# Optimization experiments

Measured on AMD Instinct MI355X. Metric: run time of the kernel, lower is better.

## Reference

```python
import jax, jax.numpy as jnp
import numpy as np
import math

B, T = 32, 64
VOCAB = 50005
EMB = 512
HID = 1024
SES = 1024
KNOW = 8785
NEG = math.exp(-100)

def _glorot(key, shape):
    fan_in, fan_out = shape[1], shape[0]
    lim = (6.0 / (fan_in + fan_out)) ** 0.5
    return jax.random.uniform(key, shape, jnp.float32, -lim, lim)

def setup_inputs() -> dict:
    key = jax.random.key(0)
    ks = jax.random.split(key, 16)
    inp = {}
    inp['ses_encoding'] = jax.random.normal(ks[0], (B, 1, SES), jnp.float32)
    inp['know_encoding'] = jax.random.normal(ks[1], (B, 1, SES), jnp.float32)
    inp['target'] = jax.random.randint(ks[2], (B, T), 0, 50000)
    inp['embed_w'] = jax.random.normal(ks[3], (VOCAB, EMB), jnp.float32) * 0.02
    # GRU params (PyTorch layout: W_ih [3H, E], W_hh [3H, H], gate order r,z,n)
    s = 1.0 / (HID ** 0.5)
    inp['W_ih'] = jax.random.uniform(ks[4], (3 * HID, EMB), jnp.float32, -s, s)
    inp['W_hh'] = jax.random.uniform(ks[5], (3 * HID, HID), jnp.float32, -s, s)
    inp['b_ih'] = jax.random.uniform(ks[6], (3 * HID,), jnp.float32, -s, s)
    inp['b_hh'] = jax.random.uniform(ks[7], (3 * HID,), jnp.float32, -s, s)
    inp['ses_to_dec_w'] = _glorot(ks[8], (HID, SES))
    inp['ses_to_dec_b'] = jnp.zeros((HID,), jnp.float32)
    inp['dec_inf_w'] = _glorot(ks[9], (2 * EMB, HID))
    inp['ses_inf_w'] = _glorot(ks[10], (2 * EMB, SES))
    inp['emb_inf_w'] = _glorot(ks[11], (2 * EMB, EMB))
    inp['emb_inf_b'] = jnp.zeros((2 * EMB,), jnp.float32)
    inp['W1'] = jax.random.normal(ks[12], (VOCAB, SES), jnp.float32) * 0.02
    inp['W2'] = jax.random.normal(ks[13], (VOCAB, SES), jnp.float32) * 0.02
    inp['W3'] = jax.random.normal(ks[14], (VOCAB, 2 * EMB), jnp.float32) * 0.02
    inp['W4'] = jax.random.normal(ks[15], (VOCAB, EMB), jnp.float32) * 0.02
    inp['know_vote_w'] = _glorot(jax.random.fold_in(key, 99), (KNOW, SES))
    return inp

def _gru_step(x, h, W_ih, W_hh, b_ih, b_hh):
    # x: [B,E], h: [B,H]
    gi = x @ W_ih.T + b_ih
    gh = h @ W_hh.T + b_hh
    ir, iz, inn = jnp.split(gi, 3, axis=-1)
    hr, hz, hn = jnp.split(gh, 3, axis=-1)
    r = jax.nn.sigmoid(ir + hr)
    z = jax.nn.sigmoid(iz + hz)
    n = jnp.tanh(inn + r * hn)
    return (1.0 - z) * h + z * n  # torch: h' = (1-z)*n + z*h with torch z; note torch formula

def _gru_step_torch(x, h, W_ih, W_hh, b_ih, b_hh):
    gi = x @ W_ih.T + b_ih
    gh = h @ W_hh.T + b_hh
    ir, iz, inn = jnp.split(gi, 3, axis=-1)
    hr, hz, hn = jnp.split(gh, 3, axis=-1)
    r = jax.nn.sigmoid(ir + hr)
    z = jax.nn.sigmoid(iz + hz)
    n = jnp.tanh(inn + r * hn)
    return (1.0 - z) * n + z * h

def reference(ses_encoding, know_encoding, target, embed_w, W_ih, W_hh, b_ih, b_hh,
              ses_to_dec_w, ses_to_dec_b, dec_inf_w, ses_inf_w, emb_inf_w, emb_inf_b,
              W1, W2, W3, W4, know_vote_w):
    ses = ses_encoding[:, 0, :]    # [B, SES]
    know = know_encoding[:, 0, :]  # [B, SES]
    target_emb = embed_w[target]   # [B, T, E]

    h0 = jnp.tanh(ses @ ses_to_dec_w.T + ses_to_dec_b)  # [B, H]

    # time-invariant pieces
    ses_inf_vec = ses @ ses_inf_w.T                      # [B, 2E]
    l1 = ses @ W1.T                                      # [B, V]
    l2 = know @ W2.T                                     # [B, V]
    # knowledge mixture log-probs (constant over time)
    ks = know @ know_vote_w.T                            # [B, KNOW]
    ks = ks[:, :-1]                                      # drop last -> [B, KNOW-1]
    pad_l = jnp.full((ks.shape[0], 10), NEG, ks.dtype)
    pad_r = jnp.full((ks.shape[0], VOCAB - 10 - (KNOW - 1)), NEG, ks.dtype)
    know_scores = jnp.concatenate([pad_l, ks, pad_r], axis=1)  # [B, V]
    know_probs = jax.nn.log_softmax(know_scores, axis=-1)      # [B, V]
    gate_const = l1 + l2                                 # [B, V]

    def step(h, emb_t):
        # emb_t: [B, E]
        h_new = _gru_step_torch(emb_t, h, W_ih, W_hh, b_ih, b_hh)  # [B, H]
        dec_hid_vec = h_new @ dec_inf_w.T                          # [B, 2E]
        target_inf = emb_t @ emb_inf_w.T + emb_inf_b               # [B, 2E]
        total = dec_hid_vec + ses_inf_vec + target_inf             # [B, 2E]
        mx = jnp.max(total.reshape(total.shape[0], EMB, 2), axis=-1)  # maxout -> [B, E]
        logits = mx @ embed_w.T                                    # shared embedding -> [B, V]
        hid_probs = jax.nn.log_softmax(logits, axis=-1)
        l3 = h_new @ W3.T                                          # note: W3 applied to hid_o [B,H]... but W3 is [V,2E]
        l4 = emb_t @ W4.T                                          # [B, V]
        gate = jax.nn.sigmoid(gate_const + l3 + l4)                # [B, V]
        final = gate * hid_probs + (1.0 - gate) * know_probs       # [B, V]
        return h_new, final

    # target_emb time-major for scan
    _, outs = jax.lax.scan(step, h0, jnp.swapaxes(target_emb, 0, 1))
    final_scores_all = jnp.swapaxes(outs, 0, 1)  # [B, T, V]
    return final_scores_all
```

## Files before the change

### kernel.cpp

```cpp
#include <hip/hip_runtime.h>

constexpr int VOC  = 50005;
constexpr int VOCP = 50048;
constexpr int VOCP2= 50176;
constexpr int NTM  = 391;
constexpr int NTMP = 400;
constexpr int KSN  = 8784;
constexpr float NPAD = 41221.0f;

typedef unsigned short u16;
typedef __attribute__((ext_vector_type(4))) float f32x4;
typedef __attribute__((ext_vector_type(8))) short bf16x8;

__device__ __forceinline__ float dot4(float4 a, float4 b) {
    return a.x*b.x + a.y*b.y + a.z*b.z + a.w*b.w;
}
__device__ __forceinline__ float sigmoidf_(float x) { return 1.0f / (1.0f + expf(-x)); }
__device__ __forceinline__ u16 f2bf(float f) {
    unsigned x = __float_as_uint(f);
    return (u16)((x + 0x7FFFu + ((x >> 16) & 1u)) >> 16);
}
__device__ __forceinline__ float bf2f(u16 u) { return __uint_as_float(((unsigned)u) << 16); }
__device__ __forceinline__ bf16x8 pack8(float4 lo, float4 hi) {
    union { bf16x8 v; unsigned u[4]; } r;
    r.u[0] = f2bf(lo.x) | ((unsigned)f2bf(lo.y) << 16);
    r.u[1] = f2bf(lo.z) | ((unsigned)f2bf(lo.w) << 16);
    r.u[2] = f2bf(hi.x) | ((unsigned)f2bf(hi.y) << 16);
    r.u[3] = f2bf(hi.z) | ((unsigned)f2bf(hi.w) << 16);
    return r.v;
}
template<int AUX>
__device__ __forceinline__ void gload_lds16x(const void* g, void* l) {
    __builtin_amdgcn_global_load_lds((const __attribute__((address_space(1))) unsigned int*)g,
                                     (__attribute__((address_space(3))) unsigned int*)l, 16, 0, AUX);
}
__device__ __forceinline__ void gload_lds16(const void* g, void* l) { gload_lds16x<0>(g, l); }
__device__ __forceinline__ void store_u16_sc(u16* p, u16 v) {
    asm volatile("global_store_short %0, %1, off sc0 sc1" :: "v"(p), "v"((unsigned)v) : "memory");
}

__global__ __launch_bounds__(256) void k_cvt(const float* __restrict__ src, u16* __restrict__ dst,
                                             int ncols, int sld, int dld) {
    int row = blockIdx.x;
    int c = (blockIdx.y * 256 + threadIdx.x) * 4;
    if (c >= ncols) return;
    float4 v = *(const float4*)(src + (size_t)row * sld + c);
    unsigned lo = f2bf(v.x) | ((unsigned)f2bf(v.y) << 16);
    unsigned hi = f2bf(v.z) | ((unsigned)f2bf(v.w) << 16);
    *(uint2*)(dst + (size_t)row * dld + c) = make_uint2(lo, hi);
}

__global__ __launch_bounds__(256) void k_pad0(u16* __restrict__ Aemb, u16* __restrict__ A34) {
    int r = VOC + blockIdx.x;
    unsigned* p3 = (unsigned*)(A34 + (size_t)r * 1536);
    for (int i = threadIdx.x; i < 768; i += 256) p3[i] = 0;
    if (r < VOCP) {
        unsigned* pe = (unsigned*)(Aemb + (size_t)r * 512);
        if (threadIdx.x < 256) pe[threadIdx.x] = 0;
    }
}

__global__ __launch_bounds__(256) void k_bsk(const float* __restrict__ ses,
                                             const float* __restrict__ know,
                                             u16* __restrict__ Bsk) {
    int row = blockIdx.x;
    for (int c0 = threadIdx.x * 4; c0 < 2048; c0 += 1024) {
        uint2 val = make_uint2(0, 0);
        if (row < 32) {
            const float* srcp = (c0 < 1024) ? ses + (size_t)row * 1024 + c0
                                            : know + (size_t)row * 1024 + (c0 - 1024);
            float4 v = *(const float4*)srcp;
            val = make_uint2(f2bf(v.x) | ((unsigned)f2bf(v.y) << 16),
                             f2bf(v.z) | ((unsigned)f2bf(v.w) << 16));
        }
        *(uint2*)(Bsk + (size_t)row * 2048 + c0) = val;
    }
}

__global__ __launch_bounds__(128) void k_gather(const float* __restrict__ embed,
                                                const int* __restrict__ target,
                                                u16* __restrict__ BG) {
    int n = blockIdx.x;
    int row = target[n];
    int c = threadIdx.x * 4;
    float4 v = *(const float4*)(embed + (size_t)row * 512 + c);
    unsigned lo = f2bf(v.x) | ((unsigned)f2bf(v.y) << 16);
    unsigned hi = f2bf(v.z) | ((unsigned)f2bf(v.w) << 16);
    *(uint2*)(BG + (size_t)n * 1536 + 1024 + c) = make_uint2(lo, hi);
}

__global__ __launch_bounds__(256) void k_h0_sesinf(const float* __restrict__ ses,
                                                   const float* __restrict__ sdw,
                                                   const float* __restrict__ sdb,
                                                   const float* __restrict__ siw,
                                                   float* __restrict__ h0,
                                                   float* __restrict__ sesinf) {
    int g = blockIdx.x * 256 + threadIdx.x;
    int b = g & 31;
    int jg = g >> 5;
    int j0 = jg * 4;
    const float4* s4 = (const float4*)(ses + (size_t)b * 1024);
    const float4* wa[4];
    const float4* wc[4];
#pragma unroll
    for (int r = 0; r < 4; ++r) {
        wa[r] = (const float4*)(sdw + (size_t)(j0 + r) * 1024);
        wc[r] = (const float4*)(siw + (size_t)(j0 + r) * 1024);
    }
    float a[4] = {0, 0, 0, 0}, c[4] = {0, 0, 0, 0};
    for (int kq = 0; kq < 256; ++kq) {
        float4 sv = s4[kq];
#pragma unroll
        for (int r = 0; r < 4; ++r) { a[r] += dot4(sv, wa[r][kq]); c[r] += dot4(sv, wc[r][kq]); }
    }
#pragma unroll
    for (int r = 0; r < 4; ++r) {
        h0[b * 1024 + j0 + r] = tanhf(a[r] + sdb[j0 + r]);
        sesinf[b * 1024 + j0 + r] = c[r];
    }
}

__global__ __launch_bounds__(256) void k_lseknow(const float* __restrict__ ks,
                                                 float* __restrict__ lsek) {
    int b = blockIdx.x;
    int t = threadIdx.x;
    __shared__ float sm[256];
    float m = -1e30f;
    for (int j = t; j < KSN; j += 256) m = fmaxf(m, ks[(size_t)b * KSN + j]);
    sm[t] = m;
    __syncthreads();
    for (int s = 128; s > 0; s >>= 1) { if (t < s) sm[t] = fmaxf(sm[t], sm[t + s]); __syncthreads(); }
    m = fmaxf(sm[0], 0.0f);
    __syncthreads();
    float s = 0.0f;
    for (int j = t; j < KSN; j += 256) s += expf(ks[(size_t)b * KSN + j] - m);
    sm[t] = s;
    __syncthreads();
    for (int r = 128; r > 0; r >>= 1) { if (t < r) sm[t] += sm[t + r]; __syncthreads(); }
    if (t == 0) lsek[b] = m + logf(sm[0] + NPAD * expf(0.0f - m));
}

template<int MODE>
__global__ __launch_bounds__(128) void k_sk32(const float* __restrict__ A1,
                                              const float* __restrict__ A2,
                                              const u16* __restrict__ Bsk,
                                              float* __restrict__ outp) {
    const int lane = threadIdx.x & 63;
    const int w = threadIdx.x >> 6;
    const int lrow = lane & 15;
    const int kg = lane >> 4;
    constexpr int K = (MODE == 0) ? 2048 : 1024;
    constexpr int bc0 = (MODE == 0) ? 0 : 1024;
    const int rowmax = (MODE == 0) ? (VOC - 1) : (KSN - 1);
    const int vb = blockIdx.x * 64 + w * 32;
    const int r0 = min(vb + lrow, rowmax);
    const int r1 = min(vb + 16 + lrow, rowmax);
    f32x4 acc[2][2] = {{{0.f,0.f,0.f,0.f},{0.f,0.f,0.f,0.f}},
                       {{0.f,0.f,0.f,0.f},{0.f,0.f,0.f,0.f}}};
    for (int k0 = 0; k0 < K; k0 += 32) {
        int kc = k0 + kg * 8;
        const float* s0;
        const float* s1;
        if (MODE == 0 && k0 >= 1024) {
            s0 = A2 + (size_t)r0 * 1024 + (kc - 1024);
            s1 = A2 + (size_t)r1 * 1024 + (kc - 1024);
        } else {
            s0 = A1 + (size_t)r0 * 1024 + kc;
            s1 = A1 + (size_t)r1 * 1024 + kc;
        }
        bf16x8 af0 = pack8(*(const float4*)s0, *(const float4*)(s0 + 4));
        bf16x8 af1 = pack8(*(const float4*)s1, *(const float4*)(s1 + 4));
        bf16x8 b0 = *(const bf16x8*)(Bsk + (size_t)lrow * 2048 + bc0 + kc);
        bf16x8 b1 = *(const bf16x8*)(Bsk + (size_t)(16 + lrow) * 2048 + bc0 + kc);
        acc[0][0] = __builtin_amdgcn_mfma_f32_16x16x32_bf16(af0, b0, acc[0][0], 0, 0, 0);
        acc[0][1] = __builtin_amdgcn_mfma_f32_16x16x32_bf16(af0, b1, acc[0][1], 0, 0, 0);
        acc[1][0] = __builtin_amdgcn_mfma_f32_16x16x32_bf16(af1, b0, acc[1][0], 0, 0, 0);
        acc[1][1] = __builtin_amdgcn_mfma_f32_16x16x32_bf16(af1, b1, acc[1][1], 0, 0, 0);
    }
    const int rg = kg * 4;
#pragma unroll
    for (int mi = 0; mi < 2; ++mi)
#pragma unroll
        for (int ni = 0; ni < 2; ++ni)
#pragma unroll
            for (int r = 0; r < 4; ++r) {
                int v = vb + mi * 16 + rg + r;
                int b = ni * 16 + lrow;
                if (MODE == 0) outp[(size_t)b * VOCP2 + v] = acc[mi][ni][r];
                else if (v < KSN) outp[(size_t)b * KSN + v] = acc[mi][ni][r];
            }
}

template<int EPI>
__global__ __launch_bounds__(256) void gemm_bt(
    const u16* __restrict__ A, int lda,
    const u16* __restrict__ B, int ldb, int K,
    const float* __restrict__ p0, const float* __restrict__ p1,
    float* __restrict__ q0, u16* __restrict__ q1, float* __restrict__ q3)
{
    __shared__ u16 Asm[128 * 64];
    __shared__ u16 Bsm[128 * 64];
    const int tid = threadIdx.x;
    const int lane = tid & 63;
    const int w = tid >> 6;
    const int wm = w >> 1, wn = w & 1;
    const int nt = blockIdx.x, mt = blockIdx.y;

    f32x4 acc[4][4];
#pragma unroll
    for (int i = 0; i < 4; ++i)
#pragma unroll
        for (int j = 0; j < 4; ++j) acc[i][j] = (f32x4){0.f, 0.f, 0.f, 0.f};

    for (int kt = 0; kt < K; kt += 64) {
#pragma unroll
        for (int p = 0; p < 4; ++p) {
            int flat = (w * 4 + p) * 64 + lane;
            int row = flat >> 3, slot = flat & 7;
            int ss = slot ^ (row & 7);
            gload_lds16(A + (size_t)(mt * 128 + row) * lda + kt + ss * 8, Asm + flat * 8);
            gload_lds16(B + (size_t)(nt * 128 + row) * ldb + kt + ss * 8, Bsm + flat * 8);
        }
        __syncthreads();
#pragma unroll
        for (int kc = 0; kc < 2; ++kc) {
            bf16x8 af[4], bfr[4];
#pragma unroll
            for (int mi = 0; mi < 4; ++mi) {
                int row = wm * 64 + mi * 16 + (lane & 15);
                int bcol = kc * 64 + ((lane >> 4) << 4);
                af[mi] = *(const bf16x8*)((const char*)Asm + row * 128 + (bcol ^ ((row & 7) << 4)));
            }
#pragma unroll
            for (int ni = 0; ni < 4; ++ni) {
                int row = wn * 64 + ni * 16 + (lane & 15);
                int bcol = kc * 64 + ((lane >> 4) << 4);
                bfr[ni] = *(const bf16x8*)((const char*)Bsm + row * 128 + (bcol ^ ((row & 7) << 4)));
            }
#pragma unroll
            for (int mi = 0; mi < 4; ++mi)
#pragma unroll
                for (int ni = 0; ni < 4; ++ni)
                    acc[mi][ni] = __builtin_amdgcn_mfma_f32_16x16x32_bf16(af[mi], bfr[ni], acc[mi][ni], 0, 0, 0);
        }
        __syncthreads();
    }

    const int cl = lane & 15;
    const int rg = (lane >> 4) << 2;

    if constexpr (EPI == 0) {
#pragma unroll
        for (int mi = 0; mi < 4; ++mi) {
            int m0 = mt * 128 + wm * 64 + mi * 16 + rg;
            float4 bias = *(const float4*)(p0 + m0);
#pragma unroll
            for (int ni = 0; ni < 4; ++ni) {
                int n = nt * 128 + wn * 64 + ni * 16 + cl;
                float4 v;
                v.x = acc[mi][ni][0] + bias.x; v.y = acc[mi][ni][1] + bias.y;
                v.z = acc[mi][ni][2] + bias.z; v.w = acc[mi][ni][3] + bias.w;
                *(float4*)(q0 + (size_t)n * 3072 + m0) = v;
            }
        }
    }
    if constexpr (EPI == 1) {
#pragma unroll
        for (int mi = 0; mi < 4; ++mi) {
            int m0 = mt * 128 + wm * 64 + mi * 16 + rg;
            float4 eb4 = *(const float4*)(p1 + m0);
#pragma unroll
            for (int ni = 0; ni < 4; ++ni) {
                int n = nt * 128 + wn * 64 + ni * 16 + cl;
                int b = n >> 6;
                float v0 = acc[mi][ni][0] + p0[b * 1024 + m0 + 0] + eb4.x;
                float v1 = acc[mi][ni][1] + p0[b * 1024 + m0 + 1] + eb4.y;
                float v2 = acc[mi][ni][2] + p0[b * 1024 + m0 + 2] + eb4.z;
                float v3 = acc[mi][ni][3] + p0[b * 1024 + m0 + 3] + eb4.w;
                unsigned pk = f2bf(fmaxf(v0, v1)) | ((unsigned)f2bf(fmaxf(v2, v3)) << 16);
                *(unsigned*)(q1 + (size_t)n * 512 + (m0 >> 1)) = pk;
            }
        }
    }
    if constexpr (EPI == 3) {
        __shared__ float redm[2][128];
        __shared__ float reds[2][128];
#pragma unroll
        for (int mi = 0; mi < 4; ++mi) {
            int v0 = mt * 128 + wm * 64 + mi * 16 + rg;
#pragma unroll
            for (int ni = 0; ni < 4; ++ni) {
                int n = nt * 128 + wn * 64 + ni * 16 + cl;
                unsigned lo = f2bf(acc[mi][ni][0]) | ((unsigned)f2bf(acc[mi][ni][1]) << 16);
                unsigned hi = f2bf(acc[mi][ni][2]) | ((unsigned)f2bf(acc[mi][ni][3]) << 16);
                *(uint2*)(q1 + (size_t)n * VOCP + v0) = make_uint2(lo, hi);
            }
        }
#pragma unroll
        for (int ni = 0; ni < 4; ++ni) {
            float lm = -1e30f;
#pragma unroll
            for (int mi = 0; mi < 4; ++mi) {
                int v0 = mt * 128 + wm * 64 + mi * 16 + rg;
#pragma unroll
                for (int r = 0; r < 4; ++r)
                    if (v0 + r < VOC) lm = fmaxf(lm, acc[mi][ni][r]);
            }
            lm = fmaxf(lm, __shfl_xor(lm, 16));
            lm = fmaxf(lm, __shfl_xor(lm, 32));
            float s = 0.0f;
#pragma unroll
            for (int mi = 0; mi < 4; ++mi) {
                int v0 = mt * 128 + wm * 64 + mi * 16 + rg;
#pragma unroll
                for (int r = 0; r < 4; ++r)
                    if (v0 + r < VOC) s += expf(acc[mi][ni][r] - lm);
            }
            s += __shfl_xor(s, 16);
            s += __shfl_xor(s, 32);
            if (lane < 16) {
                redm[wm][wn * 64 + ni * 16 + lane] = lm;
                reds[wm][wn * 64 + ni * 16 + lane] = s;
            }
        }
        __syncthreads();
        if (tid < 128) {
            float m0_ = redm[0][tid], m1_ = redm[1][tid];
            float m = fmaxf(m0_, m1_);
            float s = reds[0][tid] * expf(m0_ - m) + reds[1][tid] * expf(m1_ - m);
            int n = nt * 128 + tid;
            q0[(size_t)n * NTMP + mt] = m;
            q3[(size_t)n * NTMP + mt] = s;
        }
    }
}

__global__ __launch_bounds__(512, 1) void gemm_gate8(
    const u16* __restrict__ A,
    const u16* __restrict__ B,
    const float* __restrict__ gc2,
    unsigned char* __restrict__ g8)
{
    __shared__ __align__(16) char smem[131072];
    const int tid = threadIdx.x;
    const int lane = tid & 63;
    const int w = tid >> 6;
    const int wm = w >> 2;
    const int wn = w & 3;
    const int lrow = lane & 15;
    const int g = lane >> 4;

    int bid = blockIdx.x;
    int wg = (bid & 7) * 196 + (bid >> 3);
    int mt = wg >> 3;
    int nt = wg & 7;
    const size_t arow0 = (size_t)mt * 256;
    const size_t brow0 = (size_t)nt * 256;

    auto stageA = [&](int T, int h) {
        char* dst = smem + (T & 1) * 65536 + h * 16384;
        const u16* src = A + (arow0 + h * 128) * 1536 + T * 64;
#pragma unroll
        for (int q = 0; q < 2; ++q) {
            int flat = q * 512 + tid;
            int r = flat >> 3, s = flat & 7;
            int ss = s ^ (r & 7);
            gload_lds16(src + (size_t)r * 1536 + ss * 8, dst + flat * 16);
        }
    };
    auto stageB = [&](int T, int h) {
        char* dst = smem + (T & 1) * 65536 + 32768 + h * 16384;
        const u16* src = B + (brow0 + h * 128) * 1536 + T * 64;
#pragma unroll
        for (int q = 0; q < 2; ++q) {
            int flat = q * 512 + tid;
            int r = flat >> 3, s = flat & 7;
            int ss = s ^ (r & 7);
            gload_lds16(src + (size_t)r * 1536 + ss * 8, dst + flat * 16);
        }
    };

    f32x4 acc[8][4];
#pragma unroll
    for (int i = 0; i < 8; ++i)
#pragma unroll
        for (int j = 0; j < 4; ++j) acc[i][j] = (f32x4){0.f, 0.f, 0.f, 0.f};

    bf16x8 bf[4][2];
    auto loadB_ = [&](int d) {
        char* Bb = smem + d * 65536 + 32768 + (wn >> 1) * 16384;
#pragma unroll
        for (int ni = 0; ni < 4; ++ni) {
            int r = (wn & 1) * 64 + ni * 16 + lrow;
#pragma unroll
            for (int kk = 0; kk < 2; ++kk)
                bf[ni][kk] = *(const bf16x8*)(Bb + r * 128 + ((kk * 64 + g * 16) ^ ((r & 7) << 4)));
        }
    };

#define GPH2(D, Q, LB, STG)                                                           \
    {                                                                                 \
        STG;                                                                          \
        if (LB) loadB_(D);                                                            \
        bf16x8 af[2][2];                                                              \
        char* Ab = smem + (D) * 65536 + wm * 16384;                                   \
        _Pragma("unroll") for (int mi = 0; mi < 2; ++mi) {                            \
            int r = ((Q) * 2 + mi) * 16 + lrow;                                       \
            _Pragma("unroll") for (int kk = 0; kk < 2; ++kk)                          \
                af[mi][kk] = *(const bf16x8*)(Ab + r * 128 +                          \
                                ((kk * 64 + g * 16) ^ ((r & 7) << 4)));               \
        }                                                                             \
        asm volatile("s_waitcnt lgkmcnt(0)" ::: "memory");                            \
        __builtin_amdgcn_sched_barrier(0);                                            \
        __builtin_amdgcn_s_setprio(1);                                                \
        _Pragma("unroll") for (int kk = 0; kk < 2; ++kk)                              \
            _Pragma("unroll") for (int mi = 0; mi < 2; ++mi)                          \
                _Pragma("unroll") for (int ni = 0; ni < 4; ++ni)                      \
                    acc[(Q) * 2 + mi][ni] = __builtin_amdgcn_mfma_f32_16x16x32_bf16(  \
                        af[mi][kk], bf[ni][kk], acc[(Q) * 2 + mi][ni], 0, 0, 0);      \
        __builtin_amdgcn_s_setprio(0);                                                \
    }
#define BARR  __builtin_amdgcn_sched_barrier(0); __builtin_amdgcn_s_barrier(); \
              __builtin_amdgcn_sched_barrier(0)
#define VM4 asm volatile("s_waitcnt vmcnt(4)" ::: "memory"); __builtin_amdgcn_sched_barrier(0)
#define VM0 asm volatile("s_waitcnt vmcnt(0)" ::: "memory"); __builtin_amdgcn_sched_barrier(0)
#define NOPX (void)0

    stageB(0, 0); stageB(0, 1); stageA(0, 0); stageA(0, 1); stageB(1, 0); stageB(1, 1);
    VM4;
    BARR;

    for (int i = 0; i < 11; ++i) {
        int T0 = 2 * i, T1 = 2 * i + 1;
        GPH2(0, 0, true,  stageA(T1, 0));
        GPH2(0, 1, false, stageA(T1, 1));
        BARR;
        GPH2(0, 2, false, stageB(T0 + 2, 0));
        GPH2(0, 3, false, stageB(T0 + 2, 1));
        VM4; BARR;
        GPH2(1, 0, true,  stageA(T0 + 2, 0));
        GPH2(1, 1, false, stageA(T0 + 2, 1));
        BARR;
        GPH2(1, 2, false, stageB(T1 + 2, 0));
        GPH2(1, 3, false, stageB(T1 + 2, 1));
        VM4; BARR;
    }
    GPH2(0, 0, true,  stageA(23, 0));
    GPH2(0, 1, false, stageA(23, 1));
    BARR;
    GPH2(0, 2, false, NOPX);
    GPH2(0, 3, false, NOPX);
    VM0; BARR;
    GPH2(1, 0, true,  NOPX);
    GPH2(1, 1, false, NOPX);
    GPH2(1, 2, false, NOPX);
    GPH2(1, 3, false, NOPX);
#undef GPH2
#undef BARR
#undef VM4
#undef VM0
#undef NOPX

    const int rg = g << 2;
    const int b = nt * 4 + wn;
    const float* gcrow = gc2 + (size_t)b * VOCP2;
#pragma unroll
    for (int m = 0; m < 8; ++m) {
        int v0 = mt * 256 + wm * 128 + m * 16 + rg;
        float4 gcv = *(const float4*)(gcrow + v0);
#pragma unroll
        for (int ni = 0; ni < 4; ++ni) {
            int n = nt * 256 + wn * 64 + ni * 16 + lrow;
            unsigned pk = 0;
#pragma unroll
            for (int r = 0; r < 4; ++r) {
                float garg = acc[m][ni][r] + ((const float*)&gcv)[r];
                float gate = 1.0f / (1.0f + expf(-garg));
                pk |= ((unsigned)(int)(gate * 255.0f + 0.5f)) << (8 * r);
            }
            *(unsigned*)(g8 + (size_t)n * VOCP2 + v0) = pk;
        }
    }
}

__global__ __launch_bounds__(256, 1) void k_gru_m5(const u16* __restrict__ WhhB,
                                                   const float* __restrict__ GI,
                                                   const float* __restrict__ bhh,
                                                   const u16* __restrict__ h0b,
                                                   u16* __restrict__ BG,
                                                   unsigned* __restrict__ flags) {
    __shared__ __align__(16) char smem[163840];
    const int tid = threadIdx.x;
    const int lane = tid & 63;
    const int w = tid >> 6;
    const int jb = blockIdx.x;
    const int j0 = jb * 16;
    const int jl = tid & 15, bp = tid >> 4;
    const int je = j0 + jl;
    const float bh0 = bhh[je], bh1 = bhh[1024 + je], bh2 = bhh[2048 + je];
    char* Bbase = smem + 98304 + w * 16384;

#pragma unroll
    for (int it = 0; it < 24; ++it) {
        int flat = (it * 4 + w) * 64 + lane;
        int r = flat >> 7, s = flat & 127;
        int ss = s ^ (r & 7);
        int gr = (r >> 4) * 1024 + j0 + (r & 15);
        gload_lds16(WhhB + (size_t)gr * 1024 + ss * 8, smem + (size_t)flat * 16);
    }

    float hpv[2];
#pragma unroll
    for (int rb = 0; rb < 2; ++rb)
        hpv[rb] = bf2f(h0b[(size_t)(bp * 2 + rb) * 1024 + je]);

    const int lrow = lane & 15;
    const int ksel = lane >> 4;

    for (int t = 0; t < 64; ++t) {
        const u16* hsrc = (t == 0) ? h0b : BG + (size_t)(t - 1) * 1536;
        const size_t hstr = (t == 0) ? 1024 : (size_t)64 * 1536;

#pragma unroll
        for (int c = 0; c < 4; ++c) {
            char* dst = Bbase + c * 4096;
            int kq0 = w * 256 + c * 64;
#pragma unroll
            for (int q = 0; q < 4; ++q) {
                int flat = q * 64 + lane;
                int r = flat >> 3, s = flat & 7;
                int ss = s ^ (r & 7);
                gload_lds16x<0x11>(hsrc + (size_t)r * hstr + kq0 + ss * 8,
                                   dst + (size_t)flat * 16);
            }
        }
        float gi0[2], gi1[2], gi2[2];
#pragma unroll
        for (int rb = 0; rb < 2; ++rb) {
            const float* gp = GI + ((size_t)((bp * 2 + rb) * 64 + t)) * 3072 + je;
            gi0[rb] = gp[0]; gi1[rb] = gp[1024]; gi2[rb] = gp[2048];
        }
        if (t == 0) {
            __syncthreads();
        } else {
            asm volatile("s_waitcnt vmcnt(0)" ::: "memory");
        }
        __builtin_amdgcn_sched_barrier(0);

        f32x4 acc[3][2];
#pragma unroll
        for (int mi = 0; mi < 3; ++mi)
#pragma unroll
            for (int ni = 0; ni < 2; ++ni) acc[mi][ni] = (f32x4){0.f, 0.f, 0.f, 0.f};

#pragma unroll
        for (int c = 0; c < 4; ++c) {
            char* Bb = Bbase + c * 4096;
#pragma unroll
            for (int ks = 0; ks < 2; ++ks) {
                int kb = ks * 64 + ksel * 16;
                bf16x8 bfr[2];
#pragma unroll
                for (int ni = 0; ni < 2; ++ni) {
                    int br = ni * 16 + lrow;
                    bfr[ni] = *(const bf16x8*)(Bb + br * 128 + (kb ^ ((br & 7) << 4)));
                }
                int kA = w * 512 + c * 128 + kb;
#pragma unroll
                for (int mi = 0; mi < 3; ++mi) {
                    int ar = mi * 16 + lrow;
                    bf16x8 af = *(const bf16x8*)(smem + ar * 2048 + (kA ^ ((ar & 7) << 4)));
#pragma unroll
                    for (int ni = 0; ni < 2; ++ni)
                        acc[mi][ni] = __builtin_amdgcn_mfma_f32_16x16x32_bf16(af, bfr[ni], acc[mi][ni], 0, 0, 0);
                }
            }
        }

        float (*epiw)[33] = (float(*)[33])Bbase;
        asm volatile("s_waitcnt lgkmcnt(0)" ::: "memory");
        __builtin_amdgcn_sched_barrier(0);
        {
            const int rg = (lane >> 4) << 2;
#pragma unroll
            for (int mi = 0; mi < 3; ++mi)
#pragma unroll
                for (int ni = 0; ni < 2; ++ni) {
                    int m0 = mi * 16 + rg;
                    int cb = ni * 16 + lrow;
#pragma unroll
                    for (int r = 0; r < 4; ++r) epiw[m0 + r][cb] = acc[mi][ni][r];
                }
        }
        asm volatile("s_waitcnt lgkmcnt(0)" ::: "memory");
        __builtin_amdgcn_s_barrier();

#pragma unroll
        for (int rb = 0; rb < 2; ++rb) {
            int b = bp * 2 + rb;
            float s0 = 0.f, s1 = 0.f, s2 = 0.f;
#pragma unroll
            for (int ww = 0; ww < 4; ++ww) {
                float (*ep)[33] = (float(*)[33])(smem + 98304 + ww * 16384);
                s0 += ep[jl][b]; s1 += ep[16 + jl][b]; s2 += ep[32 + jl][b];
            }
            float rr = sigmoidf_(gi0[rb] + s0 + bh0);
            float zz = sigmoidf_(gi1[rb] + s1 + bh1);
            float nn = tanhf(gi2[rb] + rr * (s2 + bh2));
            float hnew = (1.0f - zz) * nn + zz * hpv[rb];
            hpv[rb] = hnew;
            store_u16_sc(BG + ((size_t)(b * 64 + t)) * 1536 + je, f2bf(hnew));
        }

        if (t < 63) {
            asm volatile("s_waitcnt vmcnt(0)" ::: "memory");
            __syncthreads();
            if (tid == 0)
                __hip_atomic_store(&flags[jb], (unsigned)(t + 1),
                                   __ATOMIC_RELAXED, __HIP_MEMORY_SCOPE_AGENT);
            unsigned tgt = (unsigned)(t + 1);
            while (true) {
                unsigned v = __hip_atomic_load(&flags[lane],
                                               __ATOMIC_RELAXED, __HIP_MEMORY_SCOPE_AGENT);
                if (__all(v >= tgt)) break;
                __builtin_amdgcn_s_sleep(1);
            }
            __builtin_amdgcn_sched_barrier(0);
        }
    }
}

__global__ __launch_bounds__(256) void k_lse(const float* __restrict__ pmax,
                                             const float* __restrict__ psum,
                                             float* __restrict__ lse) {
    int n = blockIdx.x;
    int t = threadIdx.x;
    __shared__ float sm[256];
    const float* pm = pmax + (size_t)n * NTMP;
    const float* ps = psum + (size_t)n * NTMP;
    float m = -1e30f;
    for (int p = t; p < NTM; p += 256) m = fmaxf(m, pm[p]);
    sm[t] = m;
    __syncthreads();
    for (int s = 128; s > 0; s >>= 1) { if (t < s) sm[t] = fmaxf(sm[t], sm[t + s]); __syncthreads(); }
    m = sm[0];
    __syncthreads();
    float s = 0.0f;
    for (int p = t; p < NTM; p += 256) s += ps[p] * expf(pm[p] - m);
    sm[t] = s;
    __syncthreads();
    for (int r = 128; r > 0; r >>= 1) { if (t < r) sm[t] += sm[t + r]; __syncthreads(); }
    if (t == 0) lse[n] = m + logf(sm[0]);
}

__global__ __launch_bounds__(256) void k_final(const u16* __restrict__ Lb,
                                               const unsigned char* __restrict__ g8,
                                               const float* __restrict__ lse,
                                               const float* __restrict__ ks,
                                               const float* __restrict__ lsek,
                                               float* __restrict__ out) {
    int n = blockIdx.y;
    int b = n >> 6;
    float lsen = lse[n], lkb = lsek[b];
    int base = blockIdx.x * 2048;
#pragma unroll
    for (int i = 0; i < 8; ++i) {
        int v = base + i * 256 + threadIdx.x;
        if (v < VOC) {
            float L = bf2f(Lb[(size_t)n * VOCP + v]);
            float g = g8[(size_t)n * VOCP2 + v] * (1.0f / 255.0f);
            float kp = ((v >= 10 && v < 10 + KSN) ? ks[(size_t)b * KSN + (v - 10)] : 0.0f) - lkb;
            out[(size_t)n * VOC + v] = g * (L - lsen) + (1.0f - g) * kp;
        }
    }
}

extern "C" void kernel_launch(void* const* d_in, const int* in_sizes, int n_in,
                              void* d_out, int out_size, void* d_ws, size_t ws_size,
                              hipStream_t stream) {
    const float* ses    = (const float*)d_in[0];
    const float* know   = (const float*)d_in[1];
    const int*   target = (const int*)d_in[2];
    const float* embed  = (const float*)d_in[3];
    const float* Wih    = (const float*)d_in[4];
    const float* Whh    = (const float*)d_in[5];
    const float* bih    = (const float*)d_in[6];
    const float* bhh    = (const float*)d_in[7];
    const float* sdw    = (const float*)d_in[8];
    const float* sdb    = (const float*)d_in[9];
    const float* dw     = (const float*)d_in[10];
    const float* siw    = (const float*)d_in[11];
    const float* ew     = (const float*)d_in[12];
    const float* eb     = (const float*)d_in[13];
    const float* W1     = (const float*)d_in[14];
    const float* W2     = (const float*)d_in[15];
    const float* W3     = (const float*)d_in[16];
    const float* W4     = (const float*)d_in[17];
    const float* kvw    = (const float*)d_in[18];

    char* ws = (char*)d_ws;
    size_t o = 0;
    auto alloc = [&](size_t bytes) { char* r = ws + o; o += (bytes + 255) & ~(size_t)255; return r; };
    u16*   Aemb  = (u16*)  alloc((size_t)VOCP * 512 * 2);
    u16*   A34   = (u16*)  alloc((size_t)VOCP2 * 1536 * 2);
    u16*   Adwew = (u16*)  alloc((size_t)1024 * 1536 * 2);
    u16*   Wihb  = (u16*)  alloc((size_t)3072 * 512 * 2);
    u16*   WhhB  = (u16*)  alloc((size_t)3072 * 1024 * 2);
    u16*   h0b   = (u16*)  alloc((size_t)32 * 1024 * 2);
    u16*   BG    = (u16*)  alloc((size_t)2048 * 1536 * 2);
    u16*   BL    = (u16*)  alloc((size_t)2048 * 512 * 2);
    float* GI    = (float*)alloc((size_t)2048 * 3072 * 4);
    float* h0    = (float*)alloc((size_t)32 * 1024 * 4);
    float* sesinf= (float*)alloc((size_t)32 * 1024 * 4);
    float* gc    = (float*)alloc((size_t)32 * VOCP2 * 4);
    float* ksb   = (float*)alloc((size_t)32 * KSN * 4);
    float* lsek  = (float*)alloc(256);
    float* lse   = (float*)alloc((size_t)2048 * 4);
    unsigned* flags = (unsigned*)alloc(256);
    float* pmax  = (float*)alloc((size_t)2048 * NTMP * 4);
    float* psum  = (float*)alloc((size_t)2048 * NTMP * 4);
    unsigned char* g8 = (unsigned char*)alloc((size_t)2048 * VOCP2);
    u16*   Lb    = (u16*)  alloc((size_t)2048 * VOCP * 2);
    u16*   Bsk   = (u16*)  alloc((size_t)128 * 2048 * 2);
    float* out = (float*)d_out;

    hipMemsetAsync(flags, 0, 256, stream);

    k_cvt<<<dim3(VOC, 1), 256, 0, stream>>>(embed, Aemb, 512, 512, 512);
    k_cvt<<<dim3(VOC, 1), 256, 0, stream>>>(W3, A34, 1024, 1024, 1536);
    k_cvt<<<dim3(VOC, 1), 256, 0, stream>>>(W4, A34 + 1024, 512, 512, 1536);
    k_pad0<<<dim3(VOCP2 - VOC), 256, 0, stream>>>(Aemb, A34);
    k_cvt<<<dim3(1024, 1), 256, 0, stream>>>(dw, Adwew, 1024, 1024, 1536);
    k_cvt<<<dim3(1024, 1), 256, 0, stream>>>(ew, Adwew + 1024, 512, 512, 1536);
    k_cvt<<<dim3(3072, 1), 256, 0, stream>>>(Wih, Wihb, 512, 512, 512);
    k_cvt<<<dim3(3072, 1), 256, 0, stream>>>(Whh, WhhB, 1024, 1024, 1024);
    k_bsk<<<dim3(128), 256, 0, stream>>>(ses, know, Bsk);

    k_gather<<<dim3(2048), 128, 0, stream>>>(embed, target, BG);
    k_h0_sesinf<<<dim3(32), 256, 0, stream>>>(ses, sdw, sdb, siw, h0, sesinf);
    k_cvt<<<dim3(32, 1), 256, 0, stream>>>(h0, h0b, 1024, 1024, 1024);

    k_sk32<0><<<dim3(VOCP2 / 64), 128, 0, stream>>>(W1, W2, Bsk, gc);
    k_sk32<1><<<dim3((KSN + 63) / 64), 128, 0, stream>>>(kvw, nullptr, Bsk, ksb);
    k_lseknow<<<dim3(32), 256, 0, stream>>>(ksb, lsek);

    gemm_bt<0><<<dim3(16, 24), 256, 0, stream>>>(Wihb, 512, BG + 1024, 1536, 512,
                                                 bih, nullptr, GI, nullptr, nullptr);
    k_gru_m5<<<dim3(64), 256, 0, stream>>>(WhhB, GI, bhh, h0b, BG, flags);
    gemm_bt<1><<<dim3(16, 8), 256, 0, stream>>>(Adwew, 1536, BG, 1536, 1536,
                                                sesinf, eb, nullptr, BL, nullptr);
    gemm_gate8<<<dim3(1568), 512, 0, stream>>>(A34, BG, gc, g8);
    gemm_bt<3><<<dim3(16, NTM), 256, 0, stream>>>(Aemb, 512, BL, 512, 512,
                                                  nullptr, nullptr, pmax, Lb, psum);
    k_lse<<<dim3(2048), 256, 0, stream>>>(pmax, psum, lse);
    k_final<<<dim3(25, 2048), 256, 0, stream>>>(Lb, g8, lse, ksb, lsek, out);
}
```

Baseline: 1.589 ms.

## Overlap vocab weight bf16 conversion with GRU recurrence using idle CUs

The separate conversion launches for embed, W3, W4, dec_inf_w and emb_inf_w, plus the padding-zero kernel, are folded into the GRU kernel. It is now launched with 256 blocks: the first 64 run the recurrence as before, and the other 192 run grid-stride fp32-to-bf16 conversion loops on CUs the latency-bound recurrence would otherwise leave idle. The goal is to hide the bandwidth-heavy conversion behind the sequential GRU. The risk is memory-bandwidth contention slowing the GRU's inter-block flag synchronisation. Each extra block also reserves the full shared-memory allocation, so co-residency depends on there being enough CUs.

```diff
diff --git a/kernel.cpp b/kernel.cpp
--- a/kernel.cpp
+++ b/kernel.cpp
@@ -38,26 +38,19 @@
 __device__ __forceinline__ void store_u16_sc(u16* p, u16 v) {
     asm volatile("global_store_short %0, %1, off sc0 sc1" :: "v"(p), "v"((unsigned)v) : "memory");
 }
+__device__ __forceinline__ void cvt4(const float* src, u16* dst) {
+    float4 v = *(const float4*)src;
+    unsigned lo = f2bf(v.x) | ((unsigned)f2bf(v.y) << 16);
+    unsigned hi = f2bf(v.z) | ((unsigned)f2bf(v.w) << 16);
+    *(uint2*)dst = make_uint2(lo, hi);
+}
 
 __global__ __launch_bounds__(256) void k_cvt(const float* __restrict__ src, u16* __restrict__ dst,
                                              int ncols, int sld, int dld) {
     int row = blockIdx.x;
     int c = (blockIdx.y * 256 + threadIdx.x) * 4;
     if (c >= ncols) return;
-    float4 v = *(const float4*)(src + (size_t)row * sld + c);
-    unsigned lo = f2bf(v.x) | ((unsigned)f2bf(v.y) << 16);
-    unsigned hi = f2bf(v.z) | ((unsigned)f2bf(v.w) << 16);
-    *(uint2*)(dst + (size_t)row * dld + c) = make_uint2(lo, hi);
-}
-
-__global__ __launch_bounds__(256) void k_pad0(u16* __restrict__ Aemb, u16* __restrict__ A34) {
-    int r = VOC + blockIdx.x;
-    unsigned* p3 = (unsigned*)(A34 + (size_t)r * 1536);
-    for (int i = threadIdx.x; i < 768; i += 256) p3[i] = 0;
-    if (r < VOCP) {
-        unsigned* pe = (unsigned*)(Aemb + (size_t)r * 512);
-        if (threadIdx.x < 256) pe[threadIdx.x] = 0;
-    }
+    cvt4(src + (size_t)row * sld + c, dst + (size_t)row * dld + c);
 }
 
 __global__ __launch_bounds__(256) void k_bsk(const float* __restrict__ ses,
@@ -83,10 +76,7 @@
     int n = blockIdx.x;
     int row = target[n];
     int c = threadIdx.x * 4;
-    float4 v = *(const float4*)(embed + (size_t)row * 512 + c);
-    unsigned lo = f2bf(v.x) | ((unsigned)f2bf(v.y) << 16);
-    unsigned hi = f2bf(v.z) | ((unsigned)f2bf(v.w) << 16);
-    *(uint2*)(BG + (size_t)n * 1536 + 1024 + c) = make_uint2(lo, hi);
+    cvt4(embed + (size_t)row * 512 + c, BG + (size_t)n * 1536 + 1024 + c);
 }
 
 __global__ __launch_bounds__(256) void k_h0_sesinf(const float* __restrict__ ses,
@@ -483,14 +473,57 @@
     }
 }
 
-__global__ __launch_bounds__(256, 1) void k_gru_m5(const u16* __restrict__ WhhB,
-                                                   const float* __restrict__ GI,
-                                                   const float* __restrict__ bhh,
-                                                   const u16* __restrict__ h0b,
-                                                   u16* __restrict__ BG,
-                                                   unsigned* __restrict__ flags) {
+__global__ __launch_bounds__(256, 1) void k_gru_f(const u16* __restrict__ WhhB,
+                                                  const float* __restrict__ GI,
+                                                  const float* __restrict__ bhh,
+                                                  const u16* __restrict__ h0b,
+                                                  u16* __restrict__ BG,
+                                                  unsigned* __restrict__ flags,
+                                                  const float* __restrict__ embed,
+                                                  const float* __restrict__ W3,
+                                                  const float* __restrict__ W4,
+                                                  const float* __restrict__ dw,
+                                                  const float* __restrict__ ew,
+                                                  u16* __restrict__ Aemb,
+                                                  u16* __restrict__ A34,
+                                                  u16* __restrict__ Adwew) {
     __shared__ __align__(16) char smem[163840];
     const int tid = threadIdx.x;
+
+    if (blockIdx.x >= 64) {
+        const long gtid = (long)(blockIdx.x - 64) * 256 + tid;
+        const long gstr = 192L * 256;
+        for (long i = gtid; i < (long)VOC * 128; i += gstr) {
+            int row = (int)(i >> 7), c4 = ((int)i & 127) * 4;
+            cvt4(embed + (size_t)row * 512 + c4, Aemb + (size_t)row * 512 + c4);
+        }
+        for (long i = gtid; i < (long)VOC * 256; i += gstr) {
+            int row = (int)(i >> 8), c4 = ((int)i & 255) * 4;
+            cvt4(W3 + (size_t)row * 1024 + c4, A34 + (size_t)row * 1536 + c4);
+        }
+        for (long i = gtid; i < (long)VOC * 128; i += gstr) {
+            int row = (int)(i >> 7), c4 = ((int)i & 127) * 4;
+            cvt4(W4 + (size_t)row * 512 + c4, A34 + (size_t)row * 1536 + 1024 + c4);
+        }
+        for (long i = gtid; i < 1024L * 256; i += gstr) {
+            int row = (int)(i >> 8), c4 = ((int)i & 255) * 4;
+            cvt4(dw + (size_t)row * 1024 + c4, Adwew + (size_t)row * 1536 + c4);
+        }
+        for (long i = gtid; i < 1024L * 128; i += gstr) {
+            int row = (int)(i >> 7), c4 = ((int)i & 127) * 4;
+            cvt4(ew + (size_t)row * 512 + c4, Adwew + (size_t)row * 1536 + 1024 + c4);
+        }
+        for (long i = gtid; i < (long)(VOCP2 - VOC) * 768; i += gstr) {
+            int row = VOC + (int)(i / 768), c = (int)(i % 768);
+            ((unsigned*)(A34 + (size_t)row * 1536))[c] = 0;
+        }
+        for (long i = gtid; i < (long)(VOCP - VOC) * 256; i += gstr) {
+            int row = VOC + (int)(i >> 8), c = (int)i & 255;
+            ((unsigned*)(Aemb + (size_t)row * 512))[c] = 0;
+        }
+        return;
+    }
+
     const int lane = tid & 63;
     const int w = tid >> 6;
     const int jb = blockIdx.x;
@@ -726,16 +759,9 @@
 
     hipMemsetAsync(flags, 0, 256, stream);
 
-    k_cvt<<<dim3(VOC, 1), 256, 0, stream>>>(embed, Aemb, 512, 512, 512);
-    k_cvt<<<dim3(VOC, 1), 256, 0, stream>>>(W3, A34, 1024, 1024, 1536);
-    k_cvt<<<dim3(VOC, 1), 256, 0, stream>>>(W4, A34 + 1024, 512, 512, 1536);
-    k_pad0<<<dim3(VOCP2 - VOC), 256, 0, stream>>>(Aemb, A34);
-    k_cvt<<<dim3(1024, 1), 256, 0, stream>>>(dw, Adwew, 1024, 1024, 1536);
-    k_cvt<<<dim3(1024, 1), 256, 0, stream>>>(ew, Adwew + 1024, 512, 512, 1536);
     k_cvt<<<dim3(3072, 1), 256, 0, stream>>>(Wih, Wihb, 512, 512, 512);
     k_cvt<<<dim3(3072, 1), 256, 0, stream>>>(Whh, WhhB, 1024, 1024, 1024);
     k_bsk<<<dim3(128), 256, 0, stream>>>(ses, know, Bsk);
-
     k_gather<<<dim3(2048), 128, 0, stream>>>(embed, target, BG);
     k_h0_sesinf<<<dim3(32), 256, 0, stream>>>(ses, sdw, sdb, siw, h0, sesinf);
     k_cvt<<<dim3(32, 1), 256, 0, stream>>>(h0, h0b, 1024, 1024, 1024);
@@ -746,7 +772,8 @@
 
     gemm_bt<0><<<dim3(16, 24), 256, 0, stream>>>(Wihb, 512, BG + 1024, 1536, 512,
                                                  bih, nullptr, GI, nullptr, nullptr);
-    k_gru_m5<<<dim3(64), 256, 0, stream>>>(WhhB, GI, bhh, h0b, BG, flags);
+    k_gru_f<<<dim3(256), 256, 0, stream>>>(WhhB, GI, bhh, h0b, BG, flags,
+                                           embed, W3, W4, dw, ew, Aemb, A34, Adwew);
     gemm_bt<1><<<dim3(16, 8), 256, 0, stream>>>(Adwew, 1536, BG, 1536, 1536,
                                                 sesinf, eb, nullptr, BL, nullptr);
     gemm_gate8<<<dim3(1568), 512, 0, stream>>>(A34, BG, gc, g8);
```

New measurement: 1.529 ms. -3.8%, faster.
